# Kernel tuning notes

Hardware: AMD Instinct MI355X
Metric: run time of the kernel (lower is better)

## Reference

```python
import jax, jax.numpy as jnp
import numpy as np

# unit constants from Converter._set_unit (astropy values, precomputed):
# unit_nu_f_nu = Lsun / (4*pi*(10 pc)^2) in erg/s/cm^2
UNIT_NU_F_NU = 3.1995e-07
# unit_f_nu = unit_nu_f_nu / (c / angstrom) in Jy
UNIT_F_NU = 1.0673e-02


def setup_inputs() -> dict:
    key = jax.random.key(0)
    k1, k2 = jax.random.split(key)
    B, F, L = 8192, 128, 8192
    # strictly increasing wavelength grid in Angstrom
    lam = 100.0 + 6.0 * (jnp.arange(L, dtype=jnp.float32) + 1.0)
    # positive fluxes so log10 is defined
    l_target = jax.random.uniform(k1, (B, L), dtype=jnp.float32) + 0.1
    # filter transmissions (already unit-normalized in __init__); keep positive
    trans_filter = 1e-3 * (jax.random.uniform(k2, (F, L), dtype=jnp.float32) + 0.01)
    return {"l_target": l_target, "trans_filter": trans_filter, "lam": lam, "return_ph": 1}


def reference(l_target, trans_filter, lam, return_ph):
    if return_ph:
        # trapz(y, x) == sum_l y[l] * w[l] with trapezoid weights w from lam.
        dx = jnp.diff(lam)  # [L-1]
        w = jnp.zeros_like(lam).at[:-1].add(0.5 * dx).at[1:].add(0.5 * dx)  # [L]
        # fuse weights into the filter matrix -> single GEMM, no [B,F,L] intermediate
        wt = trans_filter * w[None, :]  # [F, L]
        flux = jnp.einsum('bl,fl->bf', l_target, wt)  # [B, F]
        return -2.5 * jnp.log10(flux)
    else:
        return l_target * lam[None, :] * UNIT_F_NU
```

## Files before the change

kernel.cpp:

```cpp
#include <hip/hip_runtime.h>
#include <hip/hip_bf16.h>
#include <cstdint>

#define B_ROWS 8192
#define F_FILT 128
#define L_LEN  8192
#define SPLITK 16
#define KCHUNK (L_LEN / SPLITK)
#define PH_G   8
#define WAVES  8
#define BM     128
#define MBLK   (B_ROWS / BM)

typedef __attribute__((ext_vector_type(4))) float f32x4;
typedef __attribute__((ext_vector_type(8))) short bf16x8;

__device__ __forceinline__ short f2bf(float f) {
  union { float f; unsigned u; } v; v.f = f;
  unsigned u = v.u + 0x7FFFu + ((v.u >> 16) & 1u);
  return (short)(u >> 16);
}

__device__ __forceinline__ bf16x8 cvt8(f32x4 x, f32x4 y) {
  union { unsigned u[4]; bf16x8 v; } r;
  asm("v_cvt_pk_bf16_f32 %0, %1, %2" : "=v"(r.u[0]) : "v"(x[0]), "v"(x[1]));
  asm("v_cvt_pk_bf16_f32 %0, %1, %2" : "=v"(r.u[1]) : "v"(x[2]), "v"(x[3]));
  asm("v_cvt_pk_bf16_f32 %0, %1, %2" : "=v"(r.u[2]) : "v"(y[0]), "v"(y[1]));
  asm("v_cvt_pk_bf16_f32 %0, %1, %2" : "=v"(r.u[3]) : "v"(y[2]), "v"(y[3]));
  return r.v;
}

__global__ void build_wt(const float* __restrict__ trans,
                         const float* __restrict__ lam,
                         ushort* __restrict__ bp) {
  int o = blockIdx.x * blockDim.x + threadIdx.x;
  int lane = o & 63, j = (o >> 6) & 7, gs = o >> 9;
  int f = j * 16 + (lane & 15);
  int k = gs * 32 + (lane >> 4) * 8;
  bf16x8 h;
#pragma unroll
  for (int i = 0; i < 8; ++i) {
    int l = k + i;
    float lo = (l > 0)         ? lam[l - 1] : lam[0];
    float hi = (l < L_LEN - 1) ? lam[l + 1] : lam[L_LEN - 1];
    h[i] = f2bf(trans[(size_t)f * L_LEN + l] * (0.5f * (hi - lo)));
  }
  *(bf16x8*)(bp + (size_t)o * 8) = h;
}

__global__ __launch_bounds__(512, 2)
void gemm_splitk(const float* __restrict__ A,
                 const ushort* __restrict__ BP,
                 float* __restrict__ P ) {
  __shared__ ushort smem[PH_G * 8 * 64 * 8];
  const int tid  = threadIdx.x;
  const int lane = tid & 63;
  const int wave = tid >> 6;
  const int rl = lane & 15;
  const int kg = lane >> 4;
  const int m0 = blockIdx.x * BM + wave * 16;
  const int s  = blockIdx.y;
  const int k0 = s * KCHUNK;

  const uint32_t aoff = (uint32_t)(m0 + rl) * L_LEN + (uint32_t)k0 + (uint32_t)kg * 8;
  const ushort* bpc = BP + (size_t)s * 65536;

  f32x4 acc[8] = {};

  f32x4 an0 = *(const f32x4*)(A + aoff);
  f32x4 an1 = *(const f32x4*)(A + aoff + 4);
  f32x4 am0 = *(const f32x4*)(A + aoff + 32);
  f32x4 am1 = *(const f32x4*)(A + aoff + 36);

#pragma unroll
  for (int p = 0; p < 2; ++p) {
    {
      const f32x4* src = (const f32x4*)(bpc + (size_t)p * 32768);
      f32x4* dst = (f32x4*)smem;
#pragma unroll
      for (int it = 0; it < 8; ++it)
        dst[it * 512 + tid] = src[it * 512 + tid];
    }
    __syncthreads();
#pragma unroll
    for (int st = 0; st < PH_G; ++st) {
      const int ss = p * PH_G + st;
      f32x4 ac0 = an0, ac1 = an1;
      an0 = am0; an1 = am1;
      if (ss + 2 < 16) {
        am0 = *(const f32x4*)(A + aoff + (ss + 2) * 32);
        am1 = *(const f32x4*)(A + aoff + (ss + 2) * 32 + 4);
      }
      bf16x8 af = cvt8(ac0, ac1);
      const ushort* bsrc = smem + st * 4096 + lane * 8;
#pragma unroll
      for (int j = 0; j < 8; ++j) {
        bf16x8 b = *(const bf16x8*)(bsrc + j * 512);
        acc[j] = __builtin_amdgcn_mfma_f32_16x16x32_bf16(af, b, acc[j], 0, 0, 0);
      }
    }
    __syncthreads();
  }

  float* po = P + ((size_t)s * B_ROWS + m0) * F_FILT;
#pragma unroll
  for (int r = 0; r < 4; ++r) {
    const int row = kg * 4 + r;
#pragma unroll
    for (int j = 0; j < 8; ++j)
      po[(size_t)row * F_FILT + j * 16 + rl] = acc[j][r];
  }
}

__global__ void finish(const float* __restrict__ P, float* __restrict__ out) {
  int t = blockIdx.x * blockDim.x + threadIdx.x;
  f32x4 s = {};
#pragma unroll
  for (int i = 0; i < SPLITK; ++i) {
    f32x4 p = *(const f32x4*)(P + (size_t)i * ((size_t)B_ROWS * F_FILT) + (size_t)t * 4);
    s[0] += p[0]; s[1] += p[1]; s[2] += p[2]; s[3] += p[3];
  }
  f32x4 o;
  o[0] = -2.5f * log10f(s[0]);
  o[1] = -2.5f * log10f(s[1]);
  o[2] = -2.5f * log10f(s[2]);
  o[3] = -2.5f * log10f(s[3]);
  *(f32x4*)(out + (size_t)t * 4) = o;
}

extern "C" void kernel_launch(void* const* d_in, const int* in_sizes, int n_in,
                              void* d_out, int out_size, void* d_ws, size_t ws_size,
                              hipStream_t stream) {
  const float* A    = (const float*)d_in[0];
  const float* T    = (const float*)d_in[1];
  const float* lam  = (const float*)d_in[2];

  ushort* bp = (ushort*)d_ws;
  float*  P  = (float*)((char*)d_ws + (size_t)F_FILT * L_LEN * sizeof(ushort));
  float*  out = (float*)d_out;

  build_wt<<<(F_FILT * L_LEN / 8) / 256, 256, 0, stream>>>(T, lam, bp);
  gemm_splitk<<<dim3(MBLK, SPLITK), 512, 0, stream>>>(A, bp, P);
  finish<<<(B_ROWS * F_FILT / 4) / 256, 256, 0, stream>>>(P, out);
}
```

Baseline: 412.6 us.

## Stage A and B tiles into LDS via global_load_lds with smaller split-K

Rewrites the GEMM main loop to stream both the fp32 A tile and the bf16 weight tile into LDS using direct global-to-LDS loads in 16 small phases, instead of register-prefetching A and copying B through registers. Split-K is halved to 8 and occupancy target raised to 4 blocks per CU. The aim is to cut register pressure and partial-sum traffic in the finish kernel. The cost is no overlap between loads and MFMA within a block, since each phase syncs before and after compute, and LDS reads of A may hit bank conflicts.

```diff
diff --git a/kernel.cpp b/kernel.cpp
--- a/kernel.cpp
+++ b/kernel.cpp
@@ -5,10 +5,10 @@
 #define B_ROWS 8192
 #define F_FILT 128
 #define L_LEN  8192
-#define SPLITK 16
+#define SPLITK 8
 #define KCHUNK (L_LEN / SPLITK)
-#define PH_G   8
-#define WAVES  8
+#define NPH    16
+#define PH_G   2
 #define BM     128
 #define MBLK   (B_ROWS / BM)
 
@@ -30,6 +30,12 @@
   return r.v;
 }
 
+__device__ __forceinline__ void gload16(const void* g, void* l) {
+  __builtin_amdgcn_global_load_lds(
+      (const __attribute__((address_space(1))) void*)g,
+      (__attribute__((address_space(3))) void*)l, 16, 0, 0);
+}
+
 __global__ void build_wt(const float* __restrict__ trans,
                          const float* __restrict__ lam,
                          ushort* __restrict__ bp) {
@@ -48,60 +54,61 @@
   *(bf16x8*)(bp + (size_t)o * 8) = h;
 }
 
-__global__ __launch_bounds__(512, 2)
+__global__ __launch_bounds__(512, 4)
 void gemm_splitk(const float* __restrict__ A,
                  const ushort* __restrict__ BP,
                  float* __restrict__ P ) {
-  __shared__ ushort smem[PH_G * 8 * 64 * 8];
+  __shared__ float  Alds[BM * 64];
+  __shared__ ushort Blds[PH_G * 8 * 64 * 8];
+
   const int tid  = threadIdx.x;
   const int lane = tid & 63;
   const int wave = tid >> 6;
   const int rl = lane & 15;
   const int kg = lane >> 4;
-  const int m0 = blockIdx.x * BM + wave * 16;
+  const int mb = blockIdx.x * BM;
   const int s  = blockIdx.y;
-  const int k0 = s * KCHUNK;
-
-  const uint32_t aoff = (uint32_t)(m0 + rl) * L_LEN + (uint32_t)k0 + (uint32_t)kg * 8;
-  const ushort* bpc = BP + (size_t)s * 65536;
 
   f32x4 acc[8] = {};
 
-  f32x4 an0 = *(const f32x4*)(A + aoff);
-  f32x4 an1 = *(const f32x4*)(A + aoff + 4);
-  f32x4 am0 = *(const f32x4*)(A + aoff + 32);
-  f32x4 am1 = *(const f32x4*)(A + aoff + 36);
+  const int ap0 = wave * 4096 + lane * 16;
 
+  for (int ph = 0; ph < NPH; ++ph) {
+    const int ks = s * KCHUNK + ph * (PH_G * 32);
+    const int G0 = s * (KCHUNK / 32) + ph * PH_G;
 #pragma unroll
-  for (int p = 0; p < 2; ++p) {
-    {
-      const f32x4* src = (const f32x4*)(bpc + (size_t)p * 32768);
-      f32x4* dst = (f32x4*)smem;
+    for (int c = 0; c < 4; ++c) {
+      const int p = ap0 + c * 1024;
+      const int arow = p >> 8;
+      const int acol = (p & 255) >> 2;
+      gload16(A + (size_t)(mb + arow) * L_LEN + ks + acol,
+              (char*)Alds + (wave * 4 + c) * 1024);
+    }
 #pragma unroll
-      for (int it = 0; it < 8; ++it)
-        dst[it * 512 + tid] = src[it * 512 + tid];
+    for (int c = 0; c < 2; ++c) {
+      const int pb = (wave * 2 + c) * 1024 + lane * 16;
+      gload16((const char*)(BP + (size_t)G0 * 4096) + pb,
+              (char*)Blds + (wave * 2 + c) * 1024);
     }
     __syncthreads();
 #pragma unroll
-    for (int st = 0; st < PH_G; ++st) {
-      const int ss = p * PH_G + st;
-      f32x4 ac0 = an0, ac1 = an1;
-      an0 = am0; an1 = am1;
-      if (ss + 2 < 16) {
-        am0 = *(const f32x4*)(A + aoff + (ss + 2) * 32);
-        am1 = *(const f32x4*)(A + aoff + (ss + 2) * 32 + 4);
-      }
+    for (int g = 0; g < PH_G; ++g) {
+      const int row = wave * 16 + rl;
+      const char* ab = (const char*)Alds + row * 256 + g * 128 + kg * 32;
+      f32x4 ac0 = *(const f32x4*)(ab);
+      f32x4 ac1 = *(const f32x4*)(ab + 16);
       bf16x8 af = cvt8(ac0, ac1);
-      const ushort* bsrc = smem + st * 4096 + lane * 8;
+      const ushort* bb = Blds + g * 4096 + lane * 8;
 #pragma unroll
       for (int j = 0; j < 8; ++j) {
-        bf16x8 b = *(const bf16x8*)(bsrc + j * 512);
+        bf16x8 b = *(const bf16x8*)(bb + j * 512);
         acc[j] = __builtin_amdgcn_mfma_f32_16x16x32_bf16(af, b, acc[j], 0, 0, 0);
       }
     }
     __syncthreads();
   }
 
+  const int m0 = mb + wave * 16;
   float* po = P + ((size_t)s * B_ROWS + m0) * F_FILT;
 #pragma unroll
   for (int r = 0; r < 4; ++r) {
```

New measurement: 419.2 us. About the same (+1.6%).
